# Kernel tuning notes

Hardware: AMD Instinct MI355X
Metric: run time of the kernel (lower is better)

The kernel has to match this reference:

```python
import jax, jax.numpy as jnp
import numpy as np

N_MELS = 64
FRAME_RESOLUTION = 3
B, T = 8, 768
H1, H2, OUT = 128, 512, 61
NF_MAX = T // FRAME_RESOLUTION


def _rnn_dir(x, Wih, Whh, bih, bhh):
    # tanh RNN, one direction; x: [N, T, D] -> [N, T, H], h0 = 0 (as in torch)
    gx = jnp.einsum('ntd,hd->nth', x, Wih) + bih
    def step(h, g):
        h = jnp.tanh(g + h @ Whh.T + bhh)
        return h, h
    h0 = jnp.zeros((x.shape[0], Whh.shape[0]), x.dtype)
    _, hs = jax.lax.scan(step, h0, jnp.swapaxes(gx, 0, 1))
    return jnp.swapaxes(hs, 0, 1)


def _birnn(x, Wih, Whh, bih, bhh):
    # weights carry a leading direction axis [2, ...]
    f = _rnn_dir(x, Wih[0], Whh[0], bih[0], bhh[0])
    b = _rnn_dir(x[:, ::-1], Wih[1], Whh[1], bih[1], bhh[1])[:, ::-1]
    return jnp.concatenate([f, b], axis=-1)


def _gru_dir(x, Wih, Whh, bih, bhh):
    # torch GRU cell, gate order r, z, n; x: [B, F, D] -> [B, F, H]
    H = Whh.shape[-1]
    gx = jnp.einsum('bfd,gd->bfg', x, Wih) + bih
    Whr, Whz, Whn = Whh[:H], Whh[H:2 * H], Whh[2 * H:]
    bhr, bhz, bhn = bhh[:H], bhh[H:2 * H], bhh[2 * H:]
    def step(h, g):
        r = jax.nn.sigmoid(g[:, :H] + h @ Whr.T + bhr)
        z = jax.nn.sigmoid(g[:, H:2 * H] + h @ Whz.T + bhz)
        n = jnp.tanh(g[:, 2 * H:] + r * (h @ Whn.T + bhn))
        h = (1.0 - z) * n + z * h
        return h, h
    h0 = jnp.zeros((x.shape[0], H), x.dtype)
    _, hs = jax.lax.scan(step, h0, jnp.swapaxes(gx, 0, 1))
    return jnp.swapaxes(hs, 0, 1)


def _forward(batch, lengths, rnn1_Wih0, rnn1_Whh0, rnn1_bih0, rnn1_bhh0,
             rnn1_Wih1, rnn1_Whh1, rnn1_bih1, rnn1_bhh1,
             gru_Wih, gru_Whh, gru_bih, gru_bhh, fc_W, fc_b):
    Bb, Tt, M = batch.shape
    F = Tt // FRAME_RESOLUTION
    # [B, T, 64] -> frames [B*F, FR, 4 sub-bands, 16]
    frames = batch.reshape(Bb * F, FRAME_RESOLUTION, 4, 16)
    subs = []
    for j in range(4):  # fixed small loop over the 4 sub-band RNNs
        h = _birnn(frames[:, :, j, :], rnn1_Wih0[j], rnn1_Whh0[j], rnn1_bih0[j], rnn1_bhh0[j])
        h = _birnn(h, rnn1_Wih1[j], rnn1_Whh1[j], rnn1_bih1[j], rnn1_bhh1[j])
        subs.append(h[:, -1, :])  # out[:, -1, :] -> [B*F, 256]
    x = jnp.concatenate(subs, axis=-1).reshape(Bb, F, 4 * 2 * H1)  # [B, F, 1024]
    # ragged bidirectional GRU: reverse each sequence within its valid length
    nf = lengths // FRAME_RESOLUTION  # valid frames per sample
    t = jnp.arange(F)
    rev = jnp.where(t[None, :] < nf[:, None], nf[:, None] - 1 - t[None, :], t[None, :])
    for l in range(3):
        f = _gru_dir(x, gru_Wih[l, 0], gru_Whh[l, 0], gru_bih[l, 0], gru_bhh[l, 0])
        xr = jnp.take_along_axis(x, rev[:, :, None], axis=1)
        br = _gru_dir(xr, gru_Wih[l, 1], gru_Whh[l, 1], gru_bih[l, 1], gru_bhh[l, 1])
        b = jnp.take_along_axis(br, rev[:, :, None], axis=1)
        x = jnp.concatenate([f, b], axis=-1)
    return x @ fc_W.T + fc_b  # [B, F, OUT]


def setup_inputs() -> dict:
    key = jax.random.key(0)
    ks = jax.random.split(key, 16)
    s = 0.05
    batch = jax.random.normal(ks[0], (B, T, N_MELS), jnp.float32)
    nf = np.asarray(jax.random.randint(ks[1], (B,), 128, NF_MAX + 1))
    lengths = jnp.asarray(nf * FRAME_RESOLUTION, jnp.int32)  # multiples of FR
    def w(k, shape):
        return jax.random.normal(k, shape, jnp.float32) * s
    return {
        'batch': batch, 'lengths': lengths,
        'rnn1_Wih0': w(ks[2], (4, 2, H1, 16)),
        'rnn1_Whh0': w(ks[3], (4, 2, H1, H1)),
        'rnn1_bih0': w(ks[4], (4, 2, H1)),
        'rnn1_bhh0': w(ks[5], (4, 2, H1)),
        'rnn1_Wih1': w(ks[6], (4, 2, H1, 2 * H1)),
        'rnn1_Whh1': w(ks[7], (4, 2, H1, H1)),
        'rnn1_bih1': w(ks[8], (4, 2, H1)),
        'rnn1_bhh1': w(ks[9], (4, 2, H1)),
        'gru_Wih': w(ks[10], (3, 2, 3 * H2, 2 * H2)),
        'gru_Whh': w(ks[11], (3, 2, 3 * H2, H2)),
        'gru_bih': w(ks[12], (3, 2, 3 * H2)),
        'gru_bhh': w(ks[13], (3, 2, 3 * H2)),
        'fc_W': w(ks[14], (OUT, 2 * H2)),
        'fc_b': w(ks[15], (OUT,)),
    }


def reference(batch, lengths, rnn1_Wih0, rnn1_Whh0, rnn1_bih0, rnn1_bhh0,
              rnn1_Wih1, rnn1_Whh1, rnn1_bih1, rnn1_bhh1,
              gru_Wih, gru_Whh, gru_bih, gru_bhh, fc_W, fc_b):
    logits = _forward(batch, lengths, rnn1_Wih0, rnn1_Whh0, rnn1_bih0, rnn1_bhh0,
                      rnn1_Wih1, rnn1_Whh1, rnn1_bih1, rnn1_bhh1,
                      gru_Wih, gru_Whh, gru_bih, gru_bhh, fc_W, fc_b)
    # pack valid frames row-by-row: [sum(lengths)//FR, output_size]
    nf = np.asarray(lengths) // FRAME_RESOLUTION
    rows = np.repeat(np.arange(batch.shape[0]), nf)
    cols = np.concatenate([np.arange(n) for n in nf])
    return logits[rows, cols]
```

## Files before the change

### kernel.cpp

```cpp
#include <hip/hip_runtime.h>

typedef unsigned int u32;
typedef unsigned short u16;
typedef unsigned long long u64;
typedef _Float16 h2v __attribute__((ext_vector_type(2)));
typedef _Float16 f16x8 __attribute__((ext_vector_type(8)));
typedef float f32x4 __attribute__((ext_vector_type(4)));

#define DEVI static __device__ __forceinline__

DEVI u32 pack2f(float a, float b){ h2v h; h[0] = (_Float16)a; h[1] = (_Float16)b; return __builtin_bit_cast(u32, h); }
DEVI u16 f2h(float a){ _Float16 h = (_Float16)a; return __builtin_bit_cast(u16, h); }
DEVI float h2f(u16 a){ return (float)__builtin_bit_cast(_Float16, a); }

#if defined(__has_builtin)
#if __has_builtin(__builtin_amdgcn_fdot2)
#define HAVE_FDOT2 1
#endif
#endif

DEVI float dot2(u32 w, u32 x, float c){
#ifdef HAVE_FDOT2
  return __builtin_amdgcn_fdot2(__builtin_bit_cast(h2v, w), __builtin_bit_cast(h2v, x), c, false);
#else
  h2v a = __builtin_bit_cast(h2v, w), b = __builtin_bit_cast(h2v, x);
  c = fmaf((float)a[0], (float)b[0], c);
  return fmaf((float)a[1], (float)b[1], c);
#endif
}

DEVI float fsig(float x){ return 1.f / (1.f + __expf(-x)); }
DEVI float ftanh(float x){
  x = fminf(12.f, fmaxf(-12.f, x));
  float e = __expf(2.f * x);
  return (e - 1.f) / (e + 1.f);
}


__global__ void k_pack_wmfma(const float* __restrict__ W, u32* __restrict__ out){
  int idx = blockIdx.x * 256 + threadIdx.x;
  int j = idx & 3;
  int lane = (idx >> 2) & 63;
  int ng = (idx >> 8) % 192;
  int r2 = (idx >> 8) / 192;
  int kc = r2 & 31, l = r2 >> 5;
  int kq = lane >> 4, nn = lane & 15;
  int n = ng * 16 + nn;
  int kd = kc * 16 + kq * 4 + j;
  int d = (n >= 1536) ? 1 : 0;
  int g = n - d * 1536;
  const float* src = W + ((size_t)((l * 2 + d) * 1536 + g)) * 1024 + kd * 2;
  out[idx] = pack2f(src[0], src[1]);
}

__global__ void k_pack_whh(const float* __restrict__ W, u32* __restrict__ out){
  int idx = blockIdx.x * 256 + threadIdx.x;
  int kp = idx & 255;
  int q = idx >> 8;
  int g = q % 1536;
  int ld = q / 1536;
  const float* src = W + (size_t)q * 512 + kp * 2;
  int gate = g >> 9, u = g & 511;
  int w = u >> 5, uu = u & 31;
  int rr = gate * 32 + uu;
  out[(size_t)((ld * 16 + w) * 96 + rr) * 256 + kp] = pack2f(src[0], src[1]);
}

__global__ void k_pack_misc(const float* __restrict__ Wih1, const float* __restrict__ fcW,
                            const float* __restrict__ gbih, const float* __restrict__ gbhh,
                            u32* __restrict__ wp1, u32* __restrict__ fcT, float* __restrict__ BIAS){
  int idx = blockIdx.x * 256 + threadIdx.x;
  if (idx < 131072){
    int c = idx & 255; int q = idx >> 8; int kd = q & 127; int j = q >> 7;
    int d = c >> 7, i = c & 127;
    const float* src = Wih1 + ((size_t)(j * 2 + d) * 128 + i) * 256 + kd * 2;
    wp1[idx] = pack2f(src[0], src[1]);
  } else if (idx < 131072 + 32768){
    int e = idx - 131072;
    int o = e & 63, kd = e >> 6;
    u32 v = 0;
    if (o < 61) v = pack2f(fcW[o * 1024 + kd * 2], fcW[o * 1024 + kd * 2 + 1]);
    fcT[e] = v;
  } else if (idx < 131072 + 32768 + 9216){
    int e = idx - 163840;
    int l = e / 3072, n = e % 3072;
    int d = (n >= 1536) ? 1 : 0;
    int g = n - d * 1536;
    int ld = l * 2 + d;
    BIAS[e] = gbih[ld * 1536 + g] + ((g < 1024) ? gbhh[ld * 1536 + g] : 0.f);
  }
}


__global__ __launch_bounds__(256) void k_rnn1(const float* __restrict__ batch,
    const float* __restrict__ Wih0, const float* __restrict__ Whh0,
    const float* __restrict__ bih0, const float* __restrict__ bhh0,
    u16* __restrict__ y1h){
  int bid = blockIdx.x;
  int jd = bid >> 5, fb = bid & 31;
  int j = jd >> 1, d = jd & 1;
  __shared__ float Wi[16][129];
  __shared__ float Wh[128][129];
  __shared__ float hA[8][128];
  __shared__ float hB[8][128];
  __shared__ float xf[8][3][16];
  int tid = threadIdx.x;
  for (int e = tid; e < 2048; e += 256){ int i = e >> 4, k = e & 15; Wi[k][i] = Wih0[(jd * 128 + i) * 16 + k]; }
  for (int e = tid; e < 16384; e += 256){ int i = e >> 7, k = e & 127; Wh[k][i] = Whh0[(jd * 128 + i) * 128 + k]; }
  int i = tid & 127, p = tid >> 7;
  float bias = bih0[jd * 128 + i] + bhh0[jd * 128 + i];
  __syncthreads();
  for (int g8 = 0; g8 < 8; ++g8){
    int f0 = fb * 64 + g8 * 8;
    for (int e = tid; e < 384; e += 256){
      int q = e / 48, r = e % 48, t = r >> 4, k = r & 15;
      int f = f0 + q, b = f >> 8, fr = f & 255;
      xf[q][t][k] = batch[((size_t)b * 768 + fr * 3 + t) * 64 + j * 16 + k];
    }
    __syncthreads();
    int q0 = p * 4;
    for (int tt = 0; tt < 3; ++tt){
      int ta = d ? 2 - tt : tt;
      float a0 = bias, a1 = bias, a2 = bias, a3 = bias;
      #pragma unroll
      for (int k = 0; k < 16; ++k){
        float w = Wi[k][i];
        a0 = fmaf(w, xf[q0 + 0][ta][k], a0);
        a1 = fmaf(w, xf[q0 + 1][ta][k], a1);
        a2 = fmaf(w, xf[q0 + 2][ta][k], a2);
        a3 = fmaf(w, xf[q0 + 3][ta][k], a3);
      }
      if (tt > 0){
        float (*hr)[128] = (tt == 1) ? hA : hB;
        #pragma unroll 4
        for (int k = 0; k < 128; ++k){
          float w = Wh[k][i];
          a0 = fmaf(w, hr[q0 + 0][k], a0);
          a1 = fmaf(w, hr[q0 + 1][k], a1);
          a2 = fmaf(w, hr[q0 + 2][k], a2);
          a3 = fmaf(w, hr[q0 + 3][k], a3);
        }
      }
      float h0 = ftanh(a0), h1 = ftanh(a1), hh2 = ftanh(a2), h3 = ftanh(a3);
      float (*hw)[128] = (tt & 1) ? hB : hA;
      hw[q0 + 0][i] = h0; hw[q0 + 1][i] = h1; hw[q0 + 2][i] = hh2; hw[q0 + 3][i] = h3;
      size_t obase = ((size_t)(j * 2048 + f0) * 3 + ta) * 256 + d * 128 + i;
      y1h[obase + (size_t)(q0 + 0) * 768] = f2h(h0);
      y1h[obase + (size_t)(q0 + 1) * 768] = f2h(h1);
      y1h[obase + (size_t)(q0 + 2) * 768] = f2h(hh2);
      y1h[obase + (size_t)(q0 + 3) * 768] = f2h(h3);
      __syncthreads();
    }
  }
}

__global__ __launch_bounds__(256) void k_gx2(const u16* __restrict__ y1h,
    const u32* __restrict__ Wp1, const float* __restrict__ bih1,
    const float* __restrict__ bhh1, u16* __restrict__ gx2h){
  int j = blockIdx.y;
  int rt0 = blockIdx.x * 16;
  __shared__ u32 yL[16][128];
  int tid = threadIdx.x;
  const u32* y1d = (const u32*)y1h;
  for (int e = tid; e < 2048; e += 256){
    int rr = e >> 7, kd = e & 127;
    yL[rr][kd] = y1d[(size_t)(j * 6144 + rt0 + rr) * 128 + kd];
  }
  __syncthreads();
  int c = tid, d = c >> 7, i = c & 127;
  float acc[16];
  #pragma unroll
  for (int rr = 0; rr < 16; ++rr) acc[rr] = 0.f;
  const u32* wp = Wp1 + (size_t)j * 128 * 256 + c;
  for (int kd = 0; kd < 128; ++kd){
    u32 w = wp[(size_t)kd * 256];
    #pragma unroll
    for (int rr = 0; rr < 16; ++rr) acc[rr] = dot2(w, yL[rr][kd], acc[rr]);
  }
  float bias = bih1[(j * 2 + d) * 128 + i] + bhh1[(j * 2 + d) * 128 + i];
  #pragma unroll
  for (int rr = 0; rr < 16; ++rr)
    gx2h[(size_t)(j * 6144 + rt0 + rr) * 256 + c] = f2h(acc[rr] + bias);
}

__global__ __launch_bounds__(256) void k_rnn2(const u16* __restrict__ gx2h,
    const float* __restrict__ Whh1, u16* __restrict__ x0h){
  int bid = blockIdx.x;
  int j = bid >> 5, fb = bid & 31;
  __shared__ float Wh[128][129];
  __shared__ float hA[8][128];
  __shared__ float hB[8][128];
  int tid = threadIdx.x;
  for (int e = tid; e < 16384; e += 256){ int i = e >> 7, k = e & 127; Wh[k][i] = Whh1[((size_t)(j * 2) * 128 + i) * 128 + k]; }
  int i = tid & 127, p = tid >> 7, q0 = p * 4;
  __syncthreads();
  for (int g8 = 0; g8 < 8; ++g8){
    int f0 = fb * 64 + g8 * 8;
    for (int tt = 0; tt < 3; ++tt){
      float a0 = h2f(gx2h[(size_t)(j * 6144 + (f0 + q0 + 0) * 3 + tt) * 256 + i]);
      float a1 = h2f(gx2h[(size_t)(j * 6144 + (f0 + q0 + 1) * 3 + tt) * 256 + i]);
      float a2 = h2f(gx2h[(size_t)(j * 6144 + (f0 + q0 + 2) * 3 + tt) * 256 + i]);
      float a3 = h2f(gx2h[(size_t)(j * 6144 + (f0 + q0 + 3) * 3 + tt) * 256 + i]);
      if (tt > 0){
        float (*hr)[128] = (tt == 1) ? hA : hB;
        #pragma unroll 4
        for (int k = 0; k < 128; ++k){
          float w = Wh[k][i];
          a0 = fmaf(w, hr[q0 + 0][k], a0);
          a1 = fmaf(w, hr[q0 + 1][k], a1);
          a2 = fmaf(w, hr[q0 + 2][k], a2);
          a3 = fmaf(w, hr[q0 + 3][k], a3);
        }
      }
      float h0 = ftanh(a0), h1 = ftanh(a1), hh2 = ftanh(a2), h3 = ftanh(a3);
      float (*hw)[128] = (tt & 1) ? hB : hA;
      hw[q0 + 0][i] = h0; hw[q0 + 1][i] = h1; hw[q0 + 2][i] = hh2; hw[q0 + 3][i] = h3;
      if (tt == 2){
        #pragma unroll
        for (int qq = 0; qq < 4; ++qq){
          int f = f0 + q0 + qq;
          float hv = (qq == 0) ? h0 : (qq == 1) ? h1 : (qq == 2) ? hh2 : h3;
          x0h[(size_t)f * 1024 + j * 256 + i] = f2h(hv);
          float bv = ftanh(h2f(gx2h[(size_t)(j * 6144 + f * 3 + 2) * 256 + 128 + i]));
          x0h[(size_t)f * 1024 + j * 256 + 128 + i] = f2h(bv);
        }
      }
      __syncthreads();
    }
  }
}


__global__ __launch_bounds__(256) void k_gru_gxm(int l, const u16* __restrict__ xin,
    const u32* __restrict__ WB, const float* __restrict__ BIAS,
    const int* __restrict__ lengths, u16* __restrict__ gxh){
  int b = blockIdx.y >> 3, t0 = (blockIdx.y & 7) * 32;
  int nf = lengths[b] / 3;
  if (t0 >= nf) return;
  __shared__ __align__(16) u32 xL[32 * 516];
  int tid = threadIdx.x;
  const uint4* xd = (const uint4*)xin;
  for (int e = tid; e < 4096; e += 256){
    int row = e >> 7, kd4 = e & 127;
    *(uint4*)(xL + row * 516 + kd4 * 4) = xd[(size_t)(b * 256 + t0 + row) * 128 + kd4];
  }
  __syncthreads();
  int wv = tid >> 6, lane = tid & 63;
  int m0w = (wv & 1) * 16;
  int ng0 = blockIdx.x * 8 + (wv >> 1) * 4;
  const u32* aL = xL + (m0w + (lane & 15)) * 516 + (lane >> 4) * 4;
  const uint4* wb4 = (const uint4*)WB;
  f32x4 acc0 = {0.f,0.f,0.f,0.f}, acc1 = acc0, acc2 = acc0, acc3 = acc0;
  for (int kc = 0; kc < 32; ++kc){
    uint4 av = *(const uint4*)(aL + kc * 16);
    f16x8 af = __builtin_bit_cast(f16x8, av);
    const uint4* wp = wb4 + ((size_t)(l * 32 + kc) * 192 + ng0) * 64 + lane;
    uint4 b0 = wp[0], b1 = wp[64], b2 = wp[128], b3 = wp[192];
    acc0 = __builtin_amdgcn_mfma_f32_16x16x32_f16(af, __builtin_bit_cast(f16x8, b0), acc0, 0, 0, 0);
    acc1 = __builtin_amdgcn_mfma_f32_16x16x32_f16(af, __builtin_bit_cast(f16x8, b1), acc1, 0, 0, 0);
    acc2 = __builtin_amdgcn_mfma_f32_16x16x32_f16(af, __builtin_bit_cast(f16x8, b2), acc2, 0, 0, 0);
    acc3 = __builtin_amdgcn_mfma_f32_16x16x32_f16(af, __builtin_bit_cast(f16x8, b3), acc3, 0, 0, 0);
  }
  int mrow = t0 + m0w + (lane >> 4) * 4;
  #pragma unroll
  for (int sub = 0; sub < 4; ++sub){
    f32x4 ac = (sub == 0) ? acc0 : (sub == 1) ? acc1 : (sub == 2) ? acc2 : acc3;
    int n = (ng0 + sub) * 16 + (lane & 15);
    int d = (n >= 1536) ? 1 : 0;
    int g = n - d * 1536;
    float bias = BIAS[l * 3072 + n];
    u16* op = gxh + (size_t)((d * 8 + b) * 256 + mrow) * 1536 + g;
    #pragma unroll
    for (int i = 0; i < 4; ++i) op[(size_t)i * 1536] = f2h(ac[i] + bias);
  }
}

__global__ __launch_bounds__(256, 1) void k_gru_rec(int l, const u16* __restrict__ gxh,
    const float* __restrict__ gbhh, const int* __restrict__ lengths,
    const u32* __restrict__ Wr, u64* __restrict__ hpk, u16* __restrict__ xout){
  int bid = blockIdx.x;
  int w = bid & 15, b = (bid >> 4) & 7, d = bid >> 7;
  int chain = d * 8 + b;
  int nf = lengths[b] / 3;
  int tid = threadIdx.x;
  int wv = tid >> 6, lane = tid & 63;
  int hh = wv >> 1;
  int act = (wv & 1) ? (lane < 32) : 1;
  int row = (wv & 1) ? (64 + (lane & 31)) : lane;
  int u0 = w * 32;
  __shared__ __align__(16) u32 hLw[4][132];
  __shared__ float red[2][2][112];
  const uint4* wsrc = (const uint4*)(Wr + (((size_t)((l * 2 + d) * 16 + w) * 96 + row) * 256 + hh * 128));
  uint4 wreg[32];
  #pragma unroll
  for (int tt = 0; tt < 32; ++tt) wreg[tt] = wsrc[tt];
  u64* hpl = hpk + (size_t)l * 8192;
  const u16* gxb = gxh + (size_t)chain * 256 * 1536;
  float bhn = (tid < 32) ? gbhh[(l * 2 + d) * 1536 + 1024 + u0 + tid] : 0.f;
  float hprev = 0.f;
  __syncthreads();
  for (int st = 0; st < nf; ++st){
    int t = d ? (nf - 1 - st) : st;
    float gr = 0.f, gz = 0.f, gn = 0.f;
    if (tid < 32){
      const u16* gxr = gxb + (size_t)t * 1536 + u0 + tid;
      gr = h2f(gxr[0]); gz = h2f(gxr[512]); gn = h2f(gxr[1024]);
    }
    {
      u64* pb = hpl + (size_t)(st & 1) * 4096 + chain * 256 + hh * 128;
      u64 v0, v1; int gd = 0;
      do {
        v0 = __hip_atomic_load(&pb[lane], __ATOMIC_RELAXED, __HIP_MEMORY_SCOPE_AGENT);
        v1 = __hip_atomic_load(&pb[lane + 64], __ATOMIC_RELAXED, __HIP_MEMORY_SCOPE_AGENT);
      } while (((int)(v0 >> 32) < st || (int)(v1 >> 32) < st) && ++gd < (1 << 17));
      hLw[wv][lane] = (u32)v0;
      hLw[wv][lane + 64] = (u32)v1;
    }
    asm volatile("s_waitcnt lgkmcnt(0)" ::: "memory");
    __builtin_amdgcn_sched_barrier(0);
    if (act){
      float a0 = 0.f, a1 = 0.f, a2 = 0.f, a3 = 0.f;
      const u32* hb = hLw[wv];
      #pragma unroll
      for (int tt = 0; tt < 32; ++tt){
        uint4 hv = *(const uint4*)(hb + tt * 4);
        a0 = dot2(wreg[tt].x, hv.x, a0);
        a1 = dot2(wreg[tt].y, hv.y, a1);
        a2 = dot2(wreg[tt].z, hv.z, a2);
        a3 = dot2(wreg[tt].w, hv.w, a3);
      }
      red[st & 1][hh][row] = (a0 + a1) + (a2 + a3);
    }
    __syncthreads();
    float hnew = 0.f;
    if (tid < 32){
      int p = st & 1;
      float dr = red[p][0][tid]       + red[p][1][tid];
      float dz = red[p][0][tid + 32]  + red[p][1][tid + 32];
      float dn = red[p][0][tid + 64]  + red[p][1][tid + 64];
      float rg = fsig(dr + gr);
      float zg = fsig(dz + gz);
      float ng = ftanh(gn + rg * (dn + bhn));
      hnew = (1.f - zg) * ng + zg * hprev;
      hprev = hnew;
    }
    float ha = __shfl(hnew, (tid & 15) * 2);
    float hb2 = __shfl(hnew, (tid & 15) * 2 + 1);
    if (tid < 16){
      u64 v = ((u64)(u32)(st + 1) << 32) | (u64)pack2f(ha, hb2);
      __hip_atomic_store(&hpl[(size_t)((st + 1) & 1) * 4096 + chain * 256 + (u0 >> 1) + tid],
                         v, __ATOMIC_RELAXED, __HIP_MEMORY_SCOPE_AGENT);
    }
    if (tid < 32)
      xout[(size_t)(b * 256 + t) * 1024 + d * 512 + u0 + tid] = f2h(hnew);
  }
}

__global__ __launch_bounds__(256) void k_fc(const u16* __restrict__ x2h,
    const u32* __restrict__ fcT, const float* __restrict__ fcb,
    const int* __restrict__ lengths, float* __restrict__ out){
  int bid = blockIdx.x;
  int b = bid >> 5, t0 = (bid & 31) * 8;
  int nf = lengths[b] / 3;
  if (t0 >= nf) return;
  int off = 0;
  for (int b2 = 0; b2 < b; ++b2) off += lengths[b2] / 3;
  __shared__ u32 xL[512];
  __shared__ float redf[4][64];
  int tid = threadIdx.x;
  int o = tid & 63, ks = tid >> 6;
  const u32* xd = (const u32*)x2h;
  int tend = (t0 + 8 < nf) ? (t0 + 8) : nf;
  for (int t = t0; t < tend; ++t){
    for (int e = tid; e < 512; e += 256) xL[e] = xd[(size_t)(b * 256 + t) * 512 + e];
    __syncthreads();
    float acc = 0.f;
    const u32* fp = fcT + ks * 128 * 64 + o;
    #pragma unroll 4
    for (int kd = 0; kd < 128; ++kd)
      acc = dot2(fp[kd * 64], xL[ks * 128 + kd], acc);
    redf[ks][o] = acc;
    __syncthreads();
    if (ks == 0 && o < 61)
      out[(size_t)(off + t) * 61 + o] = redf[0][o] + redf[1][o] + redf[2][o] + redf[3][o] + fcb[o];
    __syncthreads();
  }
}


static constexpr size_t alignup(size_t x){ return (x + 255) & ~(size_t)255; }

extern "C" void kernel_launch(void* const* d_in, const int* in_sizes, int n_in,
                              void* d_out, int out_size, void* d_ws, size_t ws_size,
                              hipStream_t stream){
  const float* batch = (const float*)d_in[0];
  const int* lengths = (const int*)d_in[1];
  const float* Wih0 = (const float*)d_in[2];
  const float* Whh0 = (const float*)d_in[3];
  const float* bih0 = (const float*)d_in[4];
  const float* bhh0 = (const float*)d_in[5];
  const float* Wih1 = (const float*)d_in[6];
  const float* Whh1 = (const float*)d_in[7];
  const float* bih1 = (const float*)d_in[8];
  const float* bhh1 = (const float*)d_in[9];
  const float* gWih = (const float*)d_in[10];
  const float* gWhh = (const float*)d_in[11];
  const float* gbih = (const float*)d_in[12];
  const float* gbhh = (const float*)d_in[13];
  const float* fcW  = (const float*)d_in[14];
  const float* fcb  = (const float*)d_in[15];

  char* ws = (char*)d_ws;
  size_t off = 0;
  const size_t O_HPK  = off; off = alignup(off + (size_t)3 * 2 * 16 * 256 * 8);
  const size_t SYNC_BYTES = off;
  const size_t O_Y1H  = off; off = alignup(off + (size_t)4 * 2048 * 3 * 256 * 2);
  const size_t O_GX2H = off; off = alignup(off + (size_t)4 * 2048 * 3 * 256 * 2);
  const size_t O_X0   = off; off = alignup(off + (size_t)8 * 256 * 1024 * 2);
  const size_t O_X1   = off; off = alignup(off + (size_t)8 * 256 * 1024 * 2);
  const size_t O_X2   = off; off = alignup(off + (size_t)8 * 256 * 1024 * 2);
  const size_t O_GXH  = off; off = alignup(off + (size_t)2 * 8 * 256 * 1536 * 2);
  const size_t O_WBM  = off; off = alignup(off + (size_t)3 * 512 * 3072 * 4);
  const size_t O_WRH  = off; off = alignup(off + (size_t)3 * 2 * 16 * 96 * 256 * 4);
  const size_t O_WP1  = off; off = alignup(off + (size_t)4 * 128 * 256 * 4);
  const size_t O_FCT  = off; off = alignup(off + (size_t)512 * 64 * 4);
  const size_t O_BIAS = off; off = alignup(off + (size_t)3 * 3072 * 4);
  (void)ws_size; (void)in_sizes; (void)n_in; (void)out_size;

  u64* HPK  = (u64*)(ws + O_HPK);
  u16* Y1H  = (u16*)(ws + O_Y1H);
  u16* GX2H = (u16*)(ws + O_GX2H);
  u16* X0   = (u16*)(ws + O_X0);
  u16* X1   = (u16*)(ws + O_X1);
  u16* X2   = (u16*)(ws + O_X2);
  u16* GXH  = (u16*)(ws + O_GXH);
  u32* WBM  = (u32*)(ws + O_WBM);
  u32* WRH  = (u32*)(ws + O_WRH);
  u32* WP1  = (u32*)(ws + O_WP1);
  u32* FCT  = (u32*)(ws + O_FCT);
  float* BIAS = (float*)(ws + O_BIAS);

  hipMemsetAsync(ws, 0, SYNC_BYTES, stream);

  k_pack_wmfma<<<18432, 256, 0, stream>>>(gWih, WBM);
  k_pack_whh  <<<9216, 256, 0, stream>>>(gWhh, WRH);
  k_pack_misc <<<676, 256, 0, stream>>>(Wih1, fcW, gbih, gbhh, WP1, FCT, BIAS);

  k_rnn1<<<256, 256, 0, stream>>>(batch, Wih0, Whh0, bih0, bhh0, Y1H);
  k_gx2 <<<dim3(384, 4), 256, 0, stream>>>(Y1H, WP1, bih1, bhh1, GX2H);
  k_rnn2<<<128, 256, 0, stream>>>(GX2H, Whh1, X0);

  u16* X[3] = { X0, X1, X2 };
  for (int l = 0; l < 3; ++l){
    u16* xin = X[l];
    u16* xout = X[(l + 1) % 3];
    k_gru_gxm<<<dim3(24, 64), 256, 0, stream>>>(l, xin, WBM, BIAS, lengths, GXH);
    k_gru_rec<<<256, 256, 0, stream>>>(l, GXH, gbhh, lengths, WRH, HPK, xout);
  }
  k_fc<<<256, 256, 0, stream>>>(X[0], FCT, fcb, lengths, (float*)d_out);
}
```

Before: 1.629 ms.

## Interleave forward and backward GRU chains in one block per batch slice

Each recurrent GRU block now handles both directions for one batch element and hidden slice, alternating the forward and backward step inside the time loop, and the grid is halved from 256 to 128 blocks. Each block holds two sets of register-resident recurrent weights. The aim is to hide the cross-block spin-wait latency of one chain behind the compute of the other chain. The cost is double register pressure, which risks spills, plus two barriers per step and serialized work per block.

```diff
diff --git a/kernel.cpp b/kernel.cpp
--- a/kernel.cpp
+++ b/kernel.cpp
@@ -279,8 +279,8 @@
     const float* __restrict__ gbhh, const int* __restrict__ lengths,
     const u32* __restrict__ Wr, u64* __restrict__ hpk, u16* __restrict__ xout){
   int bid = blockIdx.x;
-  int w = bid & 15, b = (bid >> 4) & 7, d = bid >> 7;
-  int chain = d * 8 + b;
+  int w = bid & 15, b = bid >> 4;
+  int chA = b, chB = 8 + b;
   int nf = lengths[b] / 3;
   int tid = threadIdx.x;
   int wv = tid >> 6, lane = tid & 63;
@@ -288,71 +288,131 @@
   int act = (wv & 1) ? (lane < 32) : 1;
   int row = (wv & 1) ? (64 + (lane & 31)) : lane;
   int u0 = w * 32;
-  __shared__ __align__(16) u32 hLw[4][132];
-  __shared__ float red[2][2][112];
-  const uint4* wsrc = (const uint4*)(Wr + (((size_t)((l * 2 + d) * 16 + w) * 96 + row) * 256 + hh * 128));
-  uint4 wreg[32];
+  __shared__ __align__(16) u32 hLwA[4][132];
+  __shared__ __align__(16) u32 hLwB[4][132];
+  __shared__ float redA[2][2][112];
+  __shared__ float redB[2][2][112];
+  const uint4* wsA = (const uint4*)(Wr + (((size_t)((l * 2 + 0) * 16 + w) * 96 + row) * 256 + hh * 128));
+  const uint4* wsB = (const uint4*)(Wr + (((size_t)((l * 2 + 1) * 16 + w) * 96 + row) * 256 + hh * 128));
+  uint4 wregA[32], wregB[32];
   #pragma unroll
-  for (int tt = 0; tt < 32; ++tt) wreg[tt] = wsrc[tt];
+  for (int tt = 0; tt < 32; ++tt) wregA[tt] = wsA[tt];
+  #pragma unroll
+  for (int tt = 0; tt < 32; ++tt) wregB[tt] = wsB[tt];
   u64* hpl = hpk + (size_t)l * 8192;
-  const u16* gxb = gxh + (size_t)chain * 256 * 1536;
-  float bhn = (tid < 32) ? gbhh[(l * 2 + d) * 1536 + 1024 + u0 + tid] : 0.f;
-  float hprev = 0.f;
+  const u16* gxbA = gxh + (size_t)chA * 256 * 1536;
+  const u16* gxbB = gxh + (size_t)chB * 256 * 1536;
+  float bhnA = (tid < 32) ? gbhh[(l * 2 + 0) * 1536 + 1024 + u0 + tid] : 0.f;
+  float bhnB = (tid < 32) ? gbhh[(l * 2 + 1) * 1536 + 1024 + u0 + tid] : 0.f;
+  float hprevA = 0.f, hprevB = 0.f;
   __syncthreads();
   for (int st = 0; st < nf; ++st){
-    int t = d ? (nf - 1 - st) : st;
-    float gr = 0.f, gz = 0.f, gn = 0.f;
+    int tA = st, tB = nf - 1 - st;
+    float grA = 0.f, gzA = 0.f, gnA = 0.f, grB = 0.f, gzB = 0.f, gnB = 0.f;
     if (tid < 32){
-      const u16* gxr = gxb + (size_t)t * 1536 + u0 + tid;
-      gr = h2f(gxr[0]); gz = h2f(gxr[512]); gn = h2f(gxr[1024]);
+      const u16* ga = gxbA + (size_t)tA * 1536 + u0 + tid;
+      const u16* gb = gxbB + (size_t)tB * 1536 + u0 + tid;
+      grA = h2f(ga[0]); gzA = h2f(ga[512]); gnA = h2f(ga[1024]);
+      grB = h2f(gb[0]); gzB = h2f(gb[512]); gnB = h2f(gb[1024]);
     }
     {
-      u64* pb = hpl + (size_t)(st & 1) * 4096 + chain * 256 + hh * 128;
+      u64* pb = hpl + (size_t)(st & 1) * 4096 + chA * 256 + hh * 128;
       u64 v0, v1; int gd = 0;
       do {
         v0 = __hip_atomic_load(&pb[lane], __ATOMIC_RELAXED, __HIP_MEMORY_SCOPE_AGENT);
         v1 = __hip_atomic_load(&pb[lane + 64], __ATOMIC_RELAXED, __HIP_MEMORY_SCOPE_AGENT);
       } while (((int)(v0 >> 32) < st || (int)(v1 >> 32) < st) && ++gd < (1 << 17));
-      hLw[wv][lane] = (u32)v0;
-      hLw[wv][lane + 64] = (u32)v1;
+      hLwA[wv][lane] = (u32)v0;
+      hLwA[wv][lane + 64] = (u32)v1;
     }
     asm volatile("s_waitcnt lgkmcnt(0)" ::: "memory");
     __builtin_amdgcn_sched_barrier(0);
     if (act){
       float a0 = 0.f, a1 = 0.f, a2 = 0.f, a3 = 0.f;
-      const u32* hb = hLw[wv];
+      const u32* hb = hLwA[wv];
       #pragma unroll
       for (int tt = 0; tt < 32; ++tt){
         uint4 hv = *(const uint4*)(hb + tt * 4);
-        a0 = dot2(wreg[tt].x, hv.x, a0);
-        a1 = dot2(wreg[tt].y, hv.y, a1);
-        a2 = dot2(wreg[tt].z, hv.z, a2);
-        a3 = dot2(wreg[tt].w, hv.w, a3);
-      }
-      red[st & 1][hh][row] = (a0 + a1) + (a2 + a3);
+        a0 = dot2(wregA[tt].x, hv.x, a0);
+        a1 = dot2(wregA[tt].y, hv.y, a1);
+        a2 = dot2(wregA[tt].z, hv.z, a2);
+        a3 = dot2(wregA[tt].w, hv.w, a3);
+      }
+      redA[st & 1][hh][row] = (a0 + a1) + (a2 + a3);
     }
     __syncthreads();
-    float hnew = 0.f;
-    if (tid < 32){
-      int p = st & 1;
-      float dr = red[p][0][tid]       + red[p][1][tid];
-      float dz = red[p][0][tid + 32]  + red[p][1][tid + 32];
-      float dn = red[p][0][tid + 64]  + red[p][1][tid + 64];
-      float rg = fsig(dr + gr);
-      float zg = fsig(dz + gz);
-      float ng = ftanh(gn + rg * (dn + bhn));
-      hnew = (1.f - zg) * ng + zg * hprev;
-      hprev = hnew;
-    }
-    float ha = __shfl(hnew, (tid & 15) * 2);
-    float hb2 = __shfl(hnew, (tid & 15) * 2 + 1);
-    if (tid < 16){
-      u64 v = ((u64)(u32)(st + 1) << 32) | (u64)pack2f(ha, hb2);
-      __hip_atomic_store(&hpl[(size_t)((st + 1) & 1) * 4096 + chain * 256 + (u0 >> 1) + tid],
-                         v, __ATOMIC_RELAXED, __HIP_MEMORY_SCOPE_AGENT);
-    }
-    if (tid < 32)
-      xout[(size_t)(b * 256 + t) * 1024 + d * 512 + u0 + tid] = f2h(hnew);
+    {
+      float hnew = 0.f;
+      if (tid < 32){
+        int p = st & 1;
+        float dr = redA[p][0][tid]      + redA[p][1][tid];
+        float dz = redA[p][0][tid + 32] + redA[p][1][tid + 32];
+        float dn = redA[p][0][tid + 64] + redA[p][1][tid + 64];
+        float rg = fsig(dr + grA);
+        float zg = fsig(dz + gzA);
+        float ng = ftanh(gnA + rg * (dn + bhnA));
+        hnew = (1.f - zg) * ng + zg * hprevA;
+        hprevA = hnew;
+      }
+      float ha = __shfl(hnew, (tid & 15) * 2);
+      float hb2 = __shfl(hnew, (tid & 15) * 2 + 1);
+      if (tid < 16){
+        u64 v = ((u64)(u32)(st + 1) << 32) | (u64)pack2f(ha, hb2);
+        __hip_atomic_store(&hpl[(size_t)((st + 1) & 1) * 4096 + chA * 256 + (u0 >> 1) + tid],
+                           v, __ATOMIC_RELAXED, __HIP_MEMORY_SCOPE_AGENT);
+      }
+      if (tid < 32)
+        xout[(size_t)(b * 256 + tA) * 1024 + u0 + tid] = f2h(hnew);
+    }
+    {
+      u64* pb = hpl + (size_t)(st & 1) * 4096 + chB * 256 + hh * 128;
+      u64 v0, v1; int gd = 0;
+      do {
+        v0 = __hip_atomic_load(&pb[lane], __ATOMIC_RELAXED, __HIP_MEMORY_SCOPE_AGENT);
+        v1 = __hip_atomic_load(&pb[lane + 64], __ATOMIC_RELAXED, __HIP_MEMORY_SCOPE_AGENT);
+      } while (((int)(v0 >> 32) < st || (int)(v1 >> 32) < st) && ++gd < (1 << 17));
+      hLwB[wv][lane] = (u32)v0;
+      hLwB[wv][lane + 64] = (u32)v1;
+    }
+    asm volatile("s_waitcnt lgkmcnt(0)" ::: "memory");
+    __builtin_amdgcn_sched_barrier(0);
+    if (act){
+      float a0 = 0.f, a1 = 0.f, a2 = 0.f, a3 = 0.f;
+      const u32* hb = hLwB[wv];
+      #pragma unroll
+      for (int tt = 0; tt < 32; ++tt){
+        uint4 hv = *(const uint4*)(hb + tt * 4);
+        a0 = dot2(wregB[tt].x, hv.x, a0);
+        a1 = dot2(wregB[tt].y, hv.y, a1);
+        a2 = dot2(wregB[tt].z, hv.z, a2);
+        a3 = dot2(wregB[tt].w, hv.w, a3);
+      }
+      redB[st & 1][hh][row] = (a0 + a1) + (a2 + a3);
+    }
+    __syncthreads();
+    {
+      float hnew = 0.f;
+      if (tid < 32){
+        int p = st & 1;
+        float dr = redB[p][0][tid]      + redB[p][1][tid];
+        float dz = redB[p][0][tid + 32] + redB[p][1][tid + 32];
+        float dn = redB[p][0][tid + 64] + redB[p][1][tid + 64];
+        float rg = fsig(dr + grB);
+        float zg = fsig(dz + gzB);
+        float ng = ftanh(gnB + rg * (dn + bhnB));
+        hnew = (1.f - zg) * ng + zg * hprevB;
+        hprevB = hnew;
+      }
+      float ha = __shfl(hnew, (tid & 15) * 2);
+      float hb2 = __shfl(hnew, (tid & 15) * 2 + 1);
+      if (tid < 16){
+        u64 v = ((u64)(u32)(st + 1) << 32) | (u64)pack2f(ha, hb2);
+        __hip_atomic_store(&hpl[(size_t)((st + 1) & 1) * 4096 + chB * 256 + (u0 >> 1) + tid],
+                           v, __ATOMIC_RELAXED, __HIP_MEMORY_SCOPE_AGENT);
+      }
+      if (tid < 32)
+        xout[(size_t)(b * 256 + tB) * 1024 + 512 + u0 + tid] = f2h(hnew);
+    }
   }
 }
 
@@ -455,7 +515,7 @@
     u16* xin = X[l];
     u16* xout = X[(l + 1) % 3];
     k_gru_gxm<<<dim3(24, 64), 256, 0, stream>>>(l, xin, WBM, BIAS, lengths, GXH);
-    k_gru_rec<<<256, 256, 0, stream>>>(l, GXH, gbhh, lengths, WRH, HPK, xout);
+    k_gru_rec<<<128, 256, 0, stream>>>(l, GXH, gbhh, lengths, WRH, HPK, xout);
   }
   k_fc<<<256, 256, 0, stream>>>(X[0], FCT, fcb, lengths, (float*)d_out);
 }
```

Result: slower. 2.491 ms (+52.9%).
